# Kernel tuning notes

Hardware: AMD Instinct MI355X
Metric: run time of the kernel (lower is better)

Reference implementation:

```python
import jax, jax.numpy as jnp
import numpy as np

D_MODEL = 1024
D_K = 64
HEADS = 16


def setup_inputs() -> dict:
    key = jax.random.key(0)
    k = jax.random.split(key, 7)
    b, s = 4, 2048
    scale = 1.0 / np.sqrt(D_MODEL)
    return {
        "input_Q": jax.random.normal(k[0], (b, s, D_MODEL), jnp.float32),
        "input_K": jax.random.normal(k[1], (b, s, D_MODEL), jnp.float32),
        "input_V": jax.random.normal(k[2], (b, s, D_MODEL), jnp.float32),
        "W_Q": jax.random.normal(k[3], (D_MODEL, D_K * HEADS), jnp.float32) * scale,
        "W_K": jax.random.normal(k[4], (D_MODEL, D_K * HEADS), jnp.float32) * scale,
        "W_V": jax.random.normal(k[5], (D_MODEL, D_K * HEADS), jnp.float32) * scale,
        "W_O": jax.random.normal(k[6], (D_K * HEADS, D_MODEL), jnp.float32) * scale,
    }


def reference(input_Q, input_K, input_V, W_Q, W_K, W_V, W_O):
    b, s, _ = input_Q.shape
    # project and split heads: [b, s, h*d] -> [b, h, s, d]
    def split_heads(x):
        return x.reshape(b, -1, HEADS, D_K).transpose(0, 2, 1, 3)

    Q = split_heads(input_Q @ W_Q)
    K = split_heads(input_K @ W_K)
    V = split_heads(input_V @ W_V)

    scores = jnp.einsum("bhsd,bhtd->bhst", Q, K) / np.sqrt(D_K)  # [b,h,s,s]
    attn = jax.nn.softmax(scores, axis=-1)
    value = jnp.einsum("bhst,bhtd->bhsd", attn, V)  # [b,h,s,d]
    value = value.transpose(0, 2, 1, 3).reshape(b, s, HEADS * D_K)
    return value @ W_O
```

## Files before the change

### kernel.cpp

```cpp
#include <hip/hip_runtime.h>
#include <stdint.h>

#define DM 1024
#define HD 64
#define NH 16
#define SEQ 2048
#define NB 4

typedef __bf16 bf16x8 __attribute__((ext_vector_type(8)));
typedef __bf16 bf16x4 __attribute__((ext_vector_type(4)));
typedef float f32x4 __attribute__((ext_vector_type(4)));

#define EXP2F(x) __builtin_amdgcn_exp2f(x)

__device__ __forceinline__ float bf2f(uint16_t b) {
    uint32_t u = ((uint32_t)b) << 16;
    float f;
    __builtin_memcpy(&f, &u, 4);
    return f;
}
__device__ __forceinline__ uint16_t f2bf(float f) {
    uint32_t u;
    __builtin_memcpy(&u, &f, 4);
    u += 0x7fffu + ((u >> 16) & 1u);
    return (uint16_t)(u >> 16);
}

__device__ __forceinline__ void gll16(const void* g, void* l) {
    __builtin_amdgcn_global_load_lds(
        (const __attribute__((address_space(1))) void*)g,
        (__attribute__((address_space(3))) void*)l, 16, 0, 0);
}

__global__ __launch_bounds__(256) void cvt_f32_bf16(const float* __restrict__ in,
                                                    uint16_t* __restrict__ out) {
    const size_t i = (size_t)blockIdx.x * 256 + threadIdx.x;
    const float4* p = (const float4*)in + i * 2;
    const float4 a = p[0], b = p[1];
    uint16_t o[8] = {f2bf(a.x), f2bf(a.y), f2bf(a.z), f2bf(a.w),
                     f2bf(b.x), f2bf(b.y), f2bf(b.z), f2bf(b.w)};
    __builtin_memcpy(out + i * 8, o, 16);
}

__global__ void transpose_cvt4(const float* __restrict__ w0,
                               const float* __restrict__ w1,
                               const float* __restrict__ w2,
                               const float* __restrict__ w3,
                               uint16_t* __restrict__ o0,
                               uint16_t* __restrict__ o1,
                               uint16_t* __restrict__ o2,
                               uint16_t* __restrict__ o3) {
    __shared__ uint16_t t[32][33];
    const float* in;
    uint16_t* out;
    switch (blockIdx.z) {
        case 0: in = w0; out = o0; break;
        case 1: in = w1; out = o1; break;
        case 2: in = w2; out = o2; break;
        default: in = w3; out = o3; break;
    }
    const int bx = blockIdx.x * 32, by = blockIdx.y * 32;
    const int tx = threadIdx.x, ty = threadIdx.y;
#pragma unroll
    for (int i = ty; i < 32; i += 8)
        t[i][tx] = f2bf(in[(size_t)(by + i) * DM + bx + tx]);
    __syncthreads();
#pragma unroll
    for (int i = ty; i < 32; i += 8)
        out[(size_t)(bx + i) * DM + by + tx] = t[tx][i];
}

template <typename OT, bool TRANS>
__global__ __launch_bounds__(256) void gemm_bf16(
    const uint16_t* __restrict__ A, const uint16_t* __restrict__ Bt,
    OT* __restrict__ C, int M, int N, int K) {
    __shared__ uint16_t As[2][128 * 64];
    __shared__ uint16_t Bs[2][128 * 64];
    const int tid = threadIdx.x;
    const int wave = tid >> 6, lane = tid & 63;
    const int g = lane >> 4, l15 = lane & 15;
    const int m0 = blockIdx.y * 128, n0 = blockIdx.x * 128;
    const int wr = wave >> 1, wc = wave & 1;

    size_t aglob[4], bglob[4];
    int ldsOff[4];
#pragma unroll
    for (int i = 0; i < 4; i++) {
        const int c = wave * 4 + i;
        const int o = (c * 64 + lane) * 16;
        const int row = o >> 7, off = o & 127;
        const int soff = off ^ ((row & 7) << 4);
        aglob[i] = ((size_t)(m0 + row) * K << 1) + soff;
        bglob[i] = ((size_t)(n0 + row) * K << 1) + soff;
        ldsOff[i] = c * 1024;
    }

    f32x4 acc[4][4];
    const f32x4 z4 = {0.f, 0.f, 0.f, 0.f};
#pragma unroll
    for (int i = 0; i < 4; i++)
#pragma unroll
        for (int j = 0; j < 4; j++) acc[i][j] = z4;

#pragma unroll
    for (int i = 0; i < 4; i++) {
        gll16((const char*)A + aglob[i], (char*)As[0] + ldsOff[i]);
        gll16((const char*)Bt + bglob[i], (char*)Bs[0] + ldsOff[i]);
    }
#pragma unroll
    for (int i = 0; i < 4; i++) {
        gll16((const char*)A + aglob[i] + 128, (char*)As[1] + ldsOff[i]);
        gll16((const char*)Bt + bglob[i] + 128, (char*)Bs[1] + ldsOff[i]);
    }

    const int steps = K >> 6;
    for (int s = 0; s < steps; s++) {
        if (s + 1 < steps)
            asm volatile("s_waitcnt vmcnt(8)" ::: "memory");
        else
            asm volatile("s_waitcnt vmcnt(0)" ::: "memory");
        __builtin_amdgcn_sched_barrier(0);
        __builtin_amdgcn_s_barrier();
        __builtin_amdgcn_sched_barrier(0);

        const uint16_t* as = As[s & 1];
        const uint16_t* bs = Bs[s & 1];
#pragma unroll
        for (int ks = 0; ks < 2; ks++) {
            bf16x8 a[4], b[4];
#pragma unroll
            for (int mi = 0; mi < 4; mi++) {
                const int row = wr * 64 + mi * 16 + l15;
                a[mi] = *(const bf16x8*)((const char*)as + row * 128 +
                                         ((ks * 64 + g * 16) ^ ((row & 7) << 4)));
            }
#pragma unroll
            for (int ni = 0; ni < 4; ni++) {
                const int row = wc * 64 + ni * 16 + l15;
                b[ni] = *(const bf16x8*)((const char*)bs + row * 128 +
                                         ((ks * 64 + g * 16) ^ ((row & 7) << 4)));
            }
#pragma unroll
            for (int mi = 0; mi < 4; mi++)
#pragma unroll
                for (int ni = 0; ni < 4; ni++)
                    acc[mi][ni] = __builtin_amdgcn_mfma_f32_16x16x32_bf16(
                        a[mi], b[ni], acc[mi][ni], 0, 0, 0);
        }

        __builtin_amdgcn_sched_barrier(0);
        __builtin_amdgcn_s_barrier();
        __builtin_amdgcn_sched_barrier(0);

        if (s + 2 < steps) {
            const size_t kb = ((size_t)(s + 2) << 7);
#pragma unroll
            for (int i = 0; i < 4; i++) {
                gll16((const char*)A + aglob[i] + kb, (char*)As[s & 1] + ldsOff[i]);
                gll16((const char*)Bt + bglob[i] + kb, (char*)Bs[s & 1] + ldsOff[i]);
            }
        }
    }

    if constexpr (!TRANS) {
#pragma unroll
        for (int mi = 0; mi < 4; mi++)
#pragma unroll
            for (int ni = 0; ni < 4; ni++) {
                const int row = m0 + wr * 64 + mi * 16 + g * 4;
                const int col = n0 + wc * 64 + ni * 16 + l15;
#pragma unroll
                for (int r = 0; r < 4; r++) {
                    if constexpr (sizeof(OT) == 4)
                        C[(size_t)(row + r) * N + col] = acc[mi][ni][r];
                    else
                        C[(size_t)(row + r) * N + col] = f2bf(acc[mi][ni][r]);
                }
            }
    } else {
        char* const smb = (char*)&As[0][0];
        __syncthreads();
#pragma unroll
        for (int mi = 0; mi < 4; mi++)
#pragma unroll
            for (int ni = 0; ni < 4; ni++) {
                const int col = wc * 64 + ni * 16 + l15;
                const int row = wr * 64 + mi * 16 + g * 4;
                bf16x4 v;
                v[0] = (__bf16)acc[mi][ni][0];
                v[1] = (__bf16)acc[mi][ni][1];
                v[2] = (__bf16)acc[mi][ni][2];
                v[3] = (__bf16)acc[mi][ni][3];
                __builtin_memcpy(smb + col * 272 + row * 2, &v, 8);
            }
        __syncthreads();
        const int b0 = m0 >> 11, s0 = m0 & 2047;
        const int c = tid >> 1, half = tid & 1;
#pragma unroll
        for (int t = 0; t < 8; t++) {
            bf16x8 v;
            __builtin_memcpy(&v, smb + c * 272 + half * 128 + t * 16, 16);
            __builtin_memcpy((char*)C +
                                 (((size_t)b0 * DM + n0 + c) * SEQ + s0 +
                                  half * 64 + t * 8) * 2,
                             &v, 16);
        }
    }
}

__global__ __launch_bounds__(256, 2) void attn_fwd(
    const uint16_t* __restrict__ Q, const uint16_t* __restrict__ Kb,
    const uint16_t* __restrict__ Vt, uint16_t* __restrict__ AO) {
    __shared__ uint16_t smem[6 * 4096];
    const int tid = threadIdx.x;
    const int wave = tid >> 6, lane = tid & 63;
    const int g = lane >> 4, l15 = lane & 15;
    const int qt = blockIdx.x, h = blockIdx.y, b = blockIdx.z;
    const int q0 = qt * 256 + wave * 64;
    const int NT = SEQ / 64;
    const float SM_BIAS = 12.0f;

    uint16_t* const KsBase = smem;
    uint16_t* const VsBase = smem + 3 * 4096;

    size_t kglob[2], vglob[2];
    int ldsOff[2];
#pragma unroll
    for (int i = 0; i < 2; i++) {
        const int c = wave * 2 + i;
        const int r3 = (lane >> 3) & 7;
        const int soff = ((lane & 7) << 4) ^ (r3 << 4);
        const int kappa = (((c >> 1) & 1) << 5) | ((c & 1) << 4) |
                          (((lane >> 5) & 1) << 3) | (((c >> 2) & 1) << 2) |
                          (r3 & 3);
        kglob[i] = (((size_t)(b * SEQ + kappa) * DM + h * HD) << 1) + soff;
        vglob[i] = (((size_t)(b * DM + h * HD + c * 8 + r3) * SEQ) << 1) + soff;
        ldsOff[i] = c * 1024;
    }

    const float QSCALE = 0.125f * 1.44269504088896f;
    bf16x8 qf[4][2];
#pragma unroll
    for (int qi = 0; qi < 4; qi++)
#pragma unroll
        for (int ks = 0; ks < 2; ks++) {
            const uint16_t* src = Q + (size_t)(b * SEQ + q0 + qi * 16 + l15) * DM +
                                  h * HD + ks * 32 + g * 8;
            uint16_t tmp[8], ov[8];
            __builtin_memcpy(tmp, src, 16);
#pragma unroll
            for (int j = 0; j < 8; j++) ov[j] = f2bf(bf2f(tmp[j]) * QSCALE);
            __builtin_memcpy(&qf[qi][ks], ov, 16);
        }

    f32x4 accO[4][4];
    const f32x4 z4 = {0.f, 0.f, 0.f, 0.f};
#pragma unroll
    for (int i = 0; i < 4; i++)
#pragma unroll
        for (int j = 0; j < 4; j++) accO[i][j] = z4;
    float l_run[4] = {0.f, 0.f, 0.f, 0.f};

#pragma unroll
    for (int i = 0; i < 2; i++) {
        gll16((const char*)Kb + kglob[i], (char*)KsBase + ldsOff[i]);
        gll16((const char*)Vt + vglob[i], (char*)VsBase + ldsOff[i]);
    }
    {
        const size_t kadv = (size_t)(64 * DM * 2);
        const size_t vadv = (size_t)(64 * 2);
#pragma unroll
        for (int i = 0; i < 2; i++) {
            gll16((const char*)Kb + kglob[i] + kadv, (char*)KsBase + 8192 + ldsOff[i]);
            gll16((const char*)Vt + vglob[i] + vadv, (char*)VsBase + 8192 + ldsOff[i]);
        }
    }

    int cur = 0;
    for (int kt = 0; kt < NT; kt++) {
        if (kt + 1 < NT)
            asm volatile("s_waitcnt vmcnt(4)" ::: "memory");
        else
            asm volatile("s_waitcnt vmcnt(0)" ::: "memory");
        __builtin_amdgcn_sched_barrier(0);
        __builtin_amdgcn_s_barrier();
        __builtin_amdgcn_sched_barrier(0);

        if (kt + 2 < NT) {
            const int nb = (cur == 0) ? 2 : cur - 1;
            const size_t kadv = (size_t)(kt + 2) * (64 * DM * 2);
            const size_t vadv = (size_t)(kt + 2) * (64 * 2);
#pragma unroll
            for (int i = 0; i < 2; i++) {
                gll16((const char*)Kb + kglob[i] + kadv,
                      (char*)KsBase + nb * 8192 + ldsOff[i]);
                gll16((const char*)Vt + vglob[i] + vadv,
                      (char*)VsBase + nb * 8192 + ldsOff[i]);
            }
        }
        const uint16_t* ksrc = KsBase + cur * 4096;
        const uint16_t* vsrc = VsBase + cur * 4096;
        cur = (cur == 2) ? 0 : cur + 1;

        f32x4 sf[4][4];
        const f32x4 bias4 = {-SM_BIAS, -SM_BIAS, -SM_BIAS, -SM_BIAS};
#pragma unroll
        for (int kf = 0; kf < 4; kf++)
#pragma unroll
            for (int qi = 0; qi < 4; qi++) sf[kf][qi] = bias4;
        __builtin_amdgcn_s_setprio(1);
#pragma unroll
        for (int ks = 0; ks < 2; ks++)
#pragma unroll
            for (int kf = 0; kf < 4; kf++) {
                const int row = kf * 16 + l15;
                bf16x8 a = *(const bf16x8*)((const char*)ksrc + row * 128 +
                                            ((ks * 64 + g * 16) ^ ((row & 7) << 4)));
#pragma unroll
                for (int qi = 0; qi < 4; qi++)
                    sf[kf][qi] = __builtin_amdgcn_mfma_f32_16x16x32_bf16(
                        a, qf[qi][ks], sf[kf][qi], 0, 0, 0);
            }
        __builtin_amdgcn_s_setprio(0);

        bf16x8 pa[4][2];
#pragma unroll
        for (int qi = 0; qi < 4; qi++) {
            float ls = 0.f;
#pragma unroll
            for (int ks = 0; ks < 2; ks++) {
                bf16x8 v;
#pragma unroll
                for (int j = 0; j < 4; j++) {
                    const float p = EXP2F(sf[ks][qi][j]);
                    ls += p;
                    v[j] = (__bf16)p;
                }
#pragma unroll
                for (int j = 0; j < 4; j++) {
                    const float p = EXP2F(sf[ks + 2][qi][j]);
                    ls += p;
                    v[4 + j] = (__bf16)p;
                }
                pa[qi][ks] = v;
            }
            l_run[qi] += ls;
        }

        __builtin_amdgcn_s_setprio(1);
#pragma unroll
        for (int ks = 0; ks < 2; ks++)
#pragma unroll
            for (int nf = 0; nf < 4; nf++) {
                const int row = nf * 16 + l15;
                bf16x8 av = *(const bf16x8*)((const char*)vsrc + row * 128 +
                                             ((ks * 64 + g * 16) ^ ((row & 7) << 4)));
#pragma unroll
                for (int qi = 0; qi < 4; qi++)
                    accO[qi][nf] = __builtin_amdgcn_mfma_f32_16x16x32_bf16(
                        av, pa[qi][ks], accO[qi][nf], 0, 0, 0);
            }
        __builtin_amdgcn_s_setprio(0);
    }

    __syncthreads();

#pragma unroll
    for (int qi = 0; qi < 4; qi++) {
        l_run[qi] += __shfl_xor(l_run[qi], 16);
        l_run[qi] += __shfl_xor(l_run[qi], 32);
        l_run[qi] = 1.f / l_run[qi];
    }

    uint16_t* bw = smem + wave * 4096;
#pragma unroll
    for (int qi = 0; qi < 4; qi++) {
        const int q = qi * 16 + l15;
        const int swz = (q & 7) << 4;
#pragma unroll
        for (int nf = 0; nf < 4; nf++) {
            bf16x4 ov;
            ov[0] = (__bf16)(accO[qi][nf][0] * l_run[qi]);
            ov[1] = (__bf16)(accO[qi][nf][1] * l_run[qi]);
            ov[2] = (__bf16)(accO[qi][nf][2] * l_run[qi]);
            ov[3] = (__bf16)(accO[qi][nf][3] * l_run[qi]);
            const int off = (q * 128 + nf * 32 + g * 8) ^ swz;
            __builtin_memcpy((char*)bw + off, &ov, 8);
        }
    }
    __syncthreads();
#pragma unroll
    for (int qq = 0; qq < 2; qq++) {
        const int q = qq * 32 + (lane >> 1), part = lane & 1;
        const int swz = (q & 7) << 4;
        const size_t orow = ((size_t)(b * SEQ + q0 + q) * DM) + h * HD + part * 32;
#pragma unroll
        for (int t = 0; t < 4; t++) {
            bf16x8 ov;
            __builtin_memcpy(&ov,
                             (const char*)bw + ((q * 128 + part * 64 + t * 16) ^ swz),
                             16);
            __builtin_memcpy(&AO[orow + t * 8], &ov, 16);
        }
    }
}

extern "C" void kernel_launch(void* const* d_in, const int* in_sizes, int n_in,
                              void* d_out, int out_size, void* d_ws, size_t ws_size,
                              hipStream_t stream) {
    const float* xq = (const float*)d_in[0];
    const float* xk = (const float*)d_in[1];
    const float* xv = (const float*)d_in[2];
    const float* wq = (const float*)d_in[3];
    const float* wk = (const float*)d_in[4];
    const float* wv = (const float*)d_in[5];
    const float* wo = (const float*)d_in[6];
    float* out = (float*)d_out;
    uint16_t* ws = (uint16_t*)d_ws;

    const size_t SZ = (size_t)NB * SEQ * DM;
    const size_t WSZ = (size_t)DM * DM;
    uint16_t* bufA = ws;
    uint16_t* Qb = ws + SZ;
    uint16_t* Kbuf = ws + 2 * SZ;
    uint16_t* Vt = ws + 3 * SZ;
    uint16_t* WqT = ws + 4 * SZ;
    uint16_t* WkT = WqT + WSZ;
    uint16_t* WvT = WkT + WSZ;
    uint16_t* WoT = WvT + WSZ;

    const dim3 tb(32, 8);
    transpose_cvt4<<<dim3(32, 32, 4), tb, 0, stream>>>(wq, wk, wv, wo,
                                                       WqT, WkT, WvT, WoT);

    const int cvtBlocks = (int)(SZ / (256 * 8));
    const dim3 gg(DM / 128, NB * SEQ / 128);

    cvt_f32_bf16<<<cvtBlocks, 256, 0, stream>>>(xq, bufA);
    gemm_bf16<uint16_t, false><<<gg, 256, 0, stream>>>(bufA, WqT, Qb,
                                                       NB * SEQ, DM, DM);

    cvt_f32_bf16<<<cvtBlocks, 256, 0, stream>>>(xk, bufA);
    gemm_bf16<uint16_t, false><<<gg, 256, 0, stream>>>(bufA, WkT, Kbuf,
                                                       NB * SEQ, DM, DM);

    cvt_f32_bf16<<<cvtBlocks, 256, 0, stream>>>(xv, bufA);
    gemm_bf16<uint16_t, true><<<gg, 256, 0, stream>>>(bufA, WvT, Vt,
                                                      NB * SEQ, DM, DM);

    attn_fwd<<<dim3(SEQ / 256, NH, NB), 256, 0, stream>>>(Qb, Kbuf, Vt, bufA);

    gemm_bf16<float, false><<<dim3(DM / 128, NB * SEQ / 128), 256, 0, stream>>>(
        bufA, WoT, out, NB * SEQ, DM, DM);
}
```

Measured before the change: 223.0 us.

## Batch QKV conversions and GEMMs into single launches; MFMA-based softmax row sums

```diff
diff --git a/kernel.cpp b/kernel.cpp
--- a/kernel.cpp
+++ b/kernel.cpp
@@ -32,8 +32,17 @@
         (__attribute__((address_space(3))) void*)l, 16, 0, 0);
 }
 
-__global__ __launch_bounds__(256) void cvt_f32_bf16(const float* __restrict__ in,
-                                                    uint16_t* __restrict__ out) {
+__global__ __launch_bounds__(256) void cvt3_f32_bf16(
+    const float* __restrict__ x0, const float* __restrict__ x1,
+    const float* __restrict__ x2, uint16_t* __restrict__ o0,
+    uint16_t* __restrict__ o1, uint16_t* __restrict__ o2) {
+    const float* in;
+    uint16_t* out;
+    switch (blockIdx.z) {
+        case 0: in = x0; out = o0; break;
+        case 1: in = x1; out = o1; break;
+        default: in = x2; out = o2; break;
+    }
     const size_t i = (size_t)blockIdx.x * 256 + threadIdx.x;
     const float4* p = (const float4*)in + i * 2;
     const float4 a = p[0], b = p[1];
@@ -70,17 +79,18 @@
         out[(size_t)(bx + i) * DM + by + tx] = t[tx][i];
 }
 
-template <typename OT, bool TRANS>
-__global__ __launch_bounds__(256) void gemm_bf16(
+template <typename OT>
+__device__ __forceinline__ void gemm_body(
     const uint16_t* __restrict__ A, const uint16_t* __restrict__ Bt,
-    OT* __restrict__ C, int M, int N, int K) {
-    __shared__ uint16_t As[2][128 * 64];
-    __shared__ uint16_t Bs[2][128 * 64];
+    OT* __restrict__ C, int M, int N, int K, bool trans, uint16_t* As0,
+    uint16_t* As1, uint16_t* Bs0, uint16_t* Bs1) {
     const int tid = threadIdx.x;
     const int wave = tid >> 6, lane = tid & 63;
     const int g = lane >> 4, l15 = lane & 15;
     const int m0 = blockIdx.y * 128, n0 = blockIdx.x * 128;
     const int wr = wave >> 1, wc = wave & 1;
+    uint16_t* As[2] = {As0, As1};
+    uint16_t* Bs[2] = {Bs0, Bs1};
 
     size_t aglob[4], bglob[4];
     int ldsOff[4];
@@ -162,7 +172,7 @@
         }
     }
 
-    if constexpr (!TRANS) {
+    if (!trans) {
 #pragma unroll
         for (int mi = 0; mi < 4; mi++)
 #pragma unroll
@@ -178,7 +188,7 @@
                 }
             }
     } else {
-        char* const smb = (char*)&As[0][0];
+        char* const smb = (char*)As0;
         __syncthreads();
 #pragma unroll
         for (int mi = 0; mi < 4; mi++)
@@ -195,7 +205,7 @@
             }
         __syncthreads();
         const int b0 = m0 >> 11, s0 = m0 & 2047;
-        const int c = tid >> 1, half = tid & 1;
+        const int c = threadIdx.x >> 1, half = threadIdx.x & 1;
 #pragma unroll
         for (int t = 0; t < 8; t++) {
             bf16x8 v;
@@ -206,6 +216,33 @@
                              &v, 16);
         }
     }
+}
+
+__global__ __launch_bounds__(256) void gemm_qkv3(
+    const uint16_t* __restrict__ aq, const uint16_t* __restrict__ ak,
+    const uint16_t* __restrict__ av, const uint16_t* __restrict__ wq,
+    const uint16_t* __restrict__ wk, const uint16_t* __restrict__ wv,
+    uint16_t* __restrict__ oq, uint16_t* __restrict__ ok,
+    uint16_t* __restrict__ ov) {
+    __shared__ uint16_t As[2][128 * 64];
+    __shared__ uint16_t Bs[2][128 * 64];
+    const uint16_t *A, *Bt;
+    uint16_t* C;
+    bool trans;
+    if (blockIdx.z == 0) { A = aq; Bt = wq; C = oq; trans = false; }
+    else if (blockIdx.z == 1) { A = ak; Bt = wk; C = ok; trans = false; }
+    else { A = av; Bt = wv; C = ov; trans = true; }
+    gemm_body<uint16_t>(A, Bt, C, NB * SEQ, DM, DM, trans, As[0], As[1],
+                        Bs[0], Bs[1]);
+}
+
+__global__ __launch_bounds__(256) void gemm_out(
+    const uint16_t* __restrict__ A, const uint16_t* __restrict__ Bt,
+    float* __restrict__ C) {
+    __shared__ uint16_t As[2][128 * 64];
+    __shared__ uint16_t Bs[2][128 * 64];
+    gemm_body<float>(A, Bt, C, NB * SEQ, DM, DM, false, As[0], As[1], Bs[0],
+                     Bs[1]);
 }
 
 __global__ __launch_bounds__(256, 2) void attn_fwd(
@@ -253,13 +290,19 @@
             __builtin_memcpy(&qf[qi][ks], ov, 16);
         }
 
+    bf16x8 onesf;
+#pragma unroll
+    for (int j = 0; j < 8; j++) onesf[j] = (__bf16)1.0f;
+
     f32x4 accO[4][4];
+    f32x4 l_acc[4];
     const f32x4 z4 = {0.f, 0.f, 0.f, 0.f};
 #pragma unroll
-    for (int i = 0; i < 4; i++)
+    for (int i = 0; i < 4; i++) {
+        l_acc[i] = z4;
 #pragma unroll
         for (int j = 0; j < 4; j++) accO[i][j] = z4;
-    float l_run[4] = {0.f, 0.f, 0.f, 0.f};
+    }
 
 #pragma unroll
     for (int i = 0; i < 2; i++) {
@@ -325,31 +368,21 @@
 
         bf16x8 pa[4][2];
 #pragma unroll
-        for (int qi = 0; qi < 4; qi++) {
-            float ls = 0.f;
+        for (int qi = 0; qi < 4; qi++)
 #pragma unroll
             for (int ks = 0; ks < 2; ks++) {
                 bf16x8 v;
 #pragma unroll
                 for (int j = 0; j < 4; j++) {
-                    const float p = EXP2F(sf[ks][qi][j]);
-                    ls += p;
-                    v[j] = (__bf16)p;
-                }
-#pragma unroll
-                for (int j = 0; j < 4; j++) {
-                    const float p = EXP2F(sf[ks + 2][qi][j]);
-                    ls += p;
-                    v[4 + j] = (__bf16)p;
+                    v[j] = (__bf16)EXP2F(sf[ks][qi][j]);
+                    v[4 + j] = (__bf16)EXP2F(sf[ks + 2][qi][j]);
                 }
                 pa[qi][ks] = v;
             }
-            l_run[qi] += ls;
-        }
 
         __builtin_amdgcn_s_setprio(1);
 #pragma unroll
-        for (int ks = 0; ks < 2; ks++)
+        for (int ks = 0; ks < 2; ks++) {
 #pragma unroll
             for (int nf = 0; nf < 4; nf++) {
                 const int row = nf * 16 + l15;
@@ -360,17 +393,19 @@
                     accO[qi][nf] = __builtin_amdgcn_mfma_f32_16x16x32_bf16(
                         av, pa[qi][ks], accO[qi][nf], 0, 0, 0);
             }
+#pragma unroll
+            for (int qi = 0; qi < 4; qi++)
+                l_acc[qi] = __builtin_amdgcn_mfma_f32_16x16x32_bf16(
+                    onesf, pa[qi][ks], l_acc[qi], 0, 0, 0);
+        }
         __builtin_amdgcn_s_setprio(0);
     }
 
     __syncthreads();
 
-#pragma unroll
-    for (int qi = 0; qi < 4; qi++) {
-        l_run[qi] += __shfl_xor(l_run[qi], 16);
-        l_run[qi] += __shfl_xor(l_run[qi], 32);
-        l_run[qi] = 1.f / l_run[qi];
-    }
+    float invl[4];
+#pragma unroll
+    for (int qi = 0; qi < 4; qi++) invl[qi] = 1.f / l_acc[qi][0];
 
     uint16_t* bw = smem + wave * 4096;
 #pragma unroll
@@ -380,10 +415,10 @@
 #pragma unroll
         for (int nf = 0; nf < 4; nf++) {
             bf16x4 ov;
-            ov[0] = (__bf16)(accO[qi][nf][0] * l_run[qi]);
-            ov[1] = (__bf16)(accO[qi][nf][1] * l_run[qi]);
-            ov[2] = (__bf16)(accO[qi][nf][2] * l_run[qi]);
-            ov[3] = (__bf16)(accO[qi][nf][3] * l_run[qi]);
+            ov[0] = (__bf16)(accO[qi][nf][0] * invl[qi]);
+            ov[1] = (__bf16)(accO[qi][nf][1] * invl[qi]);
+            ov[2] = (__bf16)(accO[qi][nf][2] * invl[qi]);
+            ov[3] = (__bf16)(accO[qi][nf][3] * invl[qi]);
             const int off = (q * 128 + nf * 32 + g * 8) ^ swz;
             __builtin_memcpy((char*)bw + off, &ov, 8);
         }
@@ -420,6 +455,8 @@
 
     const size_t SZ = (size_t)NB * SEQ * DM;
     const size_t WSZ = (size_t)DM * DM;
+    uint16_t* dQ = (uint16_t*)d_out;
+    uint16_t* dK = dQ + SZ;
     uint16_t* bufA = ws;
     uint16_t* Qb = ws + SZ;
     uint16_t* Kbuf = ws + 2 * SZ;
@@ -433,23 +470,13 @@
     transpose_cvt4<<<dim3(32, 32, 4), tb, 0, stream>>>(wq, wk, wv, wo,
                                                        WqT, WkT, WvT, WoT);
 
-    const int cvtBlocks = (int)(SZ / (256 * 8));
-    const dim3 gg(DM / 128, NB * SEQ / 128);
-
-    cvt_f32_bf16<<<cvtBlocks, 256, 0, stream>>>(xq, bufA);
-    gemm_bf16<uint16_t, false><<<gg, 256, 0, stream>>>(bufA, WqT, Qb,
-                                                       NB * SEQ, DM, DM);
-
-    cvt_f32_bf16<<<cvtBlocks, 256, 0, stream>>>(xk, bufA);
-    gemm_bf16<uint16_t, false><<<gg, 256, 0, stream>>>(bufA, WkT, Kbuf,
-                                                       NB * SEQ, DM, DM);
-
-    cvt_f32_bf16<<<cvtBlocks, 256, 0, stream>>>(xv, bufA);
-    gemm_bf16<uint16_t, true><<<gg, 256, 0, stream>>>(bufA, WvT, Vt,
-                                                      NB * SEQ, DM, DM);
+    cvt3_f32_bf16<<<dim3(4096, 1, 3), 256, 0, stream>>>(xq, xk, xv,
+                                                        dQ, dK, bufA);
+
+    gemm_qkv3<<<dim3(DM / 128, NB * SEQ / 128, 3), 256, 0, stream>>>(
+        dQ, dK, bufA, WqT, WkT, WvT, Qb, Kbuf, Vt);
 
     attn_fwd<<<dim3(SEQ / 256, NH, NB), 256, 0, stream>>>(Qb, Kbuf, Vt, bufA);
 
-    gemm_bf16<float, false><<<dim3(DM / 128, NB * SEQ / 128), 256, 0, stream>>>(
-        bufA, WoT, out, NB * SEQ, DM, DM);
-}
+    gemm_out<<<dim3(DM / 128, NB * SEQ / 128), 256, 0, stream>>>(bufA, WoT, out);
+}
```

Result: no change. 221.6 us (-0.7%).
